# Optimization experiments

Hardware: AMD Instinct MI355X
Metric: run time of the kernel (lower is better)

## Reference

```python
import jax, jax.numpy as jnp
import numpy as np

E = 8          # num_experts
H = 2048       # hidden_size
I = 1408       # moe_intermediate_size
T = 4096       # tokens (batch*seq)
K = 2          # top_k


def setup_inputs() -> dict:
    key = jax.random.key(0)
    ks = jax.random.split(key, 6)
    hidden_states = jax.random.normal(ks[0], (T, H), dtype=jnp.float32)
    top_k_index = jax.random.randint(ks[1], (T, K), 0, E, dtype=jnp.int64)
    top_k_weights = jax.random.uniform(ks[2], (T, K), dtype=jnp.float32)
    scale = 0.02
    Wg = jax.random.normal(ks[3], (E, H, I), dtype=jnp.float32) * scale  # gate_proj per expert
    Wu = jax.random.normal(ks[4], (E, H, I), dtype=jnp.float32) * scale  # up_proj per expert
    Wd = jax.random.normal(ks[5], (E, I, H), dtype=jnp.float32) * scale  # down_proj per expert
    return {"hidden_states": hidden_states, "top_k_index": top_k_index,
            "top_k_weights": top_k_weights, "Wg": Wg, "Wu": Wu, "Wd": Wd}


def reference(hidden_states, top_k_index, top_k_weights, Wg, Wu, Wd):
    # Combine weights per (expert, token): w[e,t] = sum_k weights[t,k] * [idx[t,k]==e]
    one_hot = jax.nn.one_hot(top_k_index, E, dtype=hidden_states.dtype)  # [T,K,E]
    w = jnp.einsum('tke,tk->et', one_hot, top_k_weights)                 # [E,T]
    # SwiGLU MLP for every expert (dense masked-compute formulation of the
    # original gather->MLP->weighted scatter-add loop; identical math)
    g = jnp.einsum('th,ehi->eti', hidden_states, Wg)                     # [E,T,I]
    u = jnp.einsum('th,ehi->eti', hidden_states, Wu)                     # [E,T,I]
    y = jnp.einsum('eti,eih->eth', jax.nn.silu(g) * u, Wd)               # [E,T,H]
    # Weighted combine (scatter-add over experts)
    return jnp.einsum('et,eth->th', w, y)                                # [T,H]
```

## Files before the change

### kernel.cpp

```cpp
#include <hip/hip_runtime.h>

#define T_TOK 4096
#define H_DIM 2048
#define I_DIM 1408
#define E_NUM 8
#define NPAIR 8192
#define BM 128
#define BK 64

typedef float f32x4 __attribute__((ext_vector_type(4)));
typedef short s16x8 __attribute__((ext_vector_type(8)));

static __device__ __forceinline__ short f2bf(float f) {
  union { float f; unsigned u; } c; c.f = f;
  unsigned r = c.u + 0x7FFFu + ((c.u >> 16) & 1u);
  return (short)(r >> 16);
}

#define GLD16(g, l) __builtin_amdgcn_global_load_lds( \
    (const __attribute__((address_space(1))) void*)(g), \
    (__attribute__((address_space(3))) void*)(l), 16, 0, 0)

__global__ __launch_bounds__(256) void moe_build(
    const int* __restrict__ idx, const float* __restrict__ wts,
    int* __restrict__ tok_s, float* __restrict__ wt_s, int* __restrict__ inv,
    int* __restrict__ tile_e, int* __restrict__ tile_r0,
    int* __restrict__ tile_r1, int* __restrict__ ntiles) {
  __shared__ int cnt[E_NUM], cur[E_NUM];
  int tid = threadIdx.x;
  if (tid < E_NUM) cnt[tid] = 0;
  __syncthreads();
  for (int p = tid; p < NPAIR; p += 256) atomicAdd(&cnt[idx[p] & 7], 1);
  __syncthreads();
  if (tid == 0) {
    int o = 0, nt = 0;
    for (int e = 0; e < E_NUM; e++) {
      cur[e] = o;
      int c = cnt[e];
      for (int m0 = 0; m0 < c; m0 += BM) {
        tile_e[nt] = e;
        tile_r0[nt] = o + m0;
        tile_r1[nt] = o + ((m0 + BM < c) ? (m0 + BM) : c);
        nt++;
      }
      o += c;
    }
    *ntiles = nt;
  }
  __syncthreads();
  for (int p = tid; p < NPAIR; p += 256) {
    int e = idx[p] & 7;
    int pos = atomicAdd(&cur[e], 1);
    tok_s[pos] = p >> 1;
    wt_s[pos]  = wts[p];
    inv[p]     = pos;
  }
}

__global__ __launch_bounds__(256) void conv_hidden(
    const float* __restrict__ in, short* __restrict__ out) {
  size_t i = ((size_t)blockIdx.x * 256 + threadIdx.x) * 16;
  const f32x4* s = (const f32x4*)(in + i);
  f32x4 a = s[0], b = s[1], c = s[2], d = s[3];
  s16x8 v0, v1;
  v0[0]=f2bf(a[0]); v0[1]=f2bf(a[1]); v0[2]=f2bf(a[2]); v0[3]=f2bf(a[3]);
  v0[4]=f2bf(b[0]); v0[5]=f2bf(b[1]); v0[6]=f2bf(b[2]); v0[7]=f2bf(b[3]);
  v1[0]=f2bf(c[0]); v1[1]=f2bf(c[1]); v1[2]=f2bf(c[2]); v1[3]=f2bf(c[3]);
  v1[4]=f2bf(d[0]); v1[5]=f2bf(d[1]); v1[6]=f2bf(d[2]); v1[7]=f2bf(d[3]);
  *(s16x8*)(out + i) = v0;
  *(s16x8*)(out + i + 8) = v1;
}

__global__ __launch_bounds__(256) void transpose_w(
    const float* __restrict__ in, short* __restrict__ out, int R, int C) {
  __shared__ short t[64][72];
  const float* src = in + (size_t)blockIdx.z * ((size_t)R * C);
  short* dst = out + (size_t)blockIdx.z * ((size_t)R * C);
  int r0 = blockIdx.y * 64, c0 = blockIdx.x * 64;
  int tid = threadIdx.x;
  int ir = tid >> 2, ic = (tid & 3) * 16;
  const f32x4* s = (const f32x4*)(src + (size_t)(r0 + ir) * C + c0 + ic);
  f32x4 a = s[0], b = s[1], c = s[2], d = s[3];
  short* w = &t[ir][ic];
  w[0]=f2bf(a[0]);  w[1]=f2bf(a[1]);  w[2]=f2bf(a[2]);  w[3]=f2bf(a[3]);
  w[4]=f2bf(b[0]);  w[5]=f2bf(b[1]);  w[6]=f2bf(b[2]);  w[7]=f2bf(b[3]);
  w[8]=f2bf(c[0]);  w[9]=f2bf(c[1]);  w[10]=f2bf(c[2]); w[11]=f2bf(c[3]);
  w[12]=f2bf(d[0]); w[13]=f2bf(d[1]); w[14]=f2bf(d[2]); w[15]=f2bf(d[3]);
  __syncthreads();
  int oc = tid >> 2, os = (tid & 3) * 16;
  s16x8 v0, v1;
  #pragma unroll
  for (int j = 0; j < 8; j++) { v0[j] = t[os + j][oc]; v1[j] = t[os + 8 + j][oc]; }
  short* o = dst + (size_t)(c0 + oc) * R + r0 + os;
  *(s16x8*)o = v0;
  *(s16x8*)(o + 8) = v1;
}

__global__ __launch_bounds__(256, 2) void moe_gemm1(
    const short* __restrict__ hb, const short* __restrict__ Wgt,
    const short* __restrict__ Wut, const int* __restrict__ tok_s,
    const int* __restrict__ tile_e, const int* __restrict__ tile_r0,
    const int* __restrict__ tile_r1, const int* __restrict__ ntiles,
    short* __restrict__ act) {
  __shared__ short As[BM * BK];
  __shared__ short Bg[128 * BK];
  __shared__ short Bu[128 * BK];
  int bt = blockIdx.x;
  if (bt >= *ntiles) return;
  int e = tile_e[bt], r0 = tile_r0[bt], r1 = tile_r1[bt];
  int n0 = blockIdx.y * 128;
  const short* wg = Wgt + (size_t)e * ((size_t)H_DIM * I_DIM);
  const short* wu = Wut + (size_t)e * ((size_t)H_DIM * I_DIM);

  int tid = threadIdx.x, lane = tid & 63, wv = tid >> 6;
  int l3 = lane >> 3;
  int k8 = (((lane & 7) ^ l3) << 3);

  const short* a_src[4]; short* a_dst[4];
  const short* g_src[4]; short* g_dst[4];
  const short* u_src[4]; short* u_dst[4];
  #pragma unroll
  for (int s = 0; s < 4; s++) {
    int row = wv * 32 + s * 8 + l3;
    int p = r0 + row; if (p > NPAIR - 1) p = NPAIR - 1;
    a_src[s] = hb + (size_t)tok_s[p] * H_DIM + k8;
    a_dst[s] = As + (wv * 32 + s * 8) * BK;
    g_src[s] = wg + (size_t)(n0 + row) * H_DIM + k8;
    u_src[s] = wu + (size_t)(n0 + row) * H_DIM + k8;
    g_dst[s] = Bg + (wv * 32 + s * 8) * BK;
    u_dst[s] = Bu + (wv * 32 + s * 8) * BK;
  }

  int wm = wv >> 1, wn = wv & 1;
  int lrow = lane & 15, lk = lane >> 4;

  f32x4 accg[4][4], accu[4][4];
  #pragma unroll
  for (int i = 0; i < 4; i++)
    #pragma unroll
    for (int j = 0; j < 4; j++) { accg[i][j] = 0; accu[i][j] = 0; }

  for (int k0 = 0; k0 < H_DIM; k0 += BK) {
    #pragma unroll
    for (int s = 0; s < 4; s++) GLD16(a_src[s] + k0, a_dst[s]);
    #pragma unroll
    for (int s = 0; s < 4; s++) GLD16(g_src[s] + k0, g_dst[s]);
    #pragma unroll
    for (int s = 0; s < 4; s++) GLD16(u_src[s] + k0, u_dst[s]);
    __syncthreads();
    #pragma unroll
    for (int ks = 0; ks < 2; ks++) {
      s16x8 af[4], bgf[4], buf_[4];
      #pragma unroll
      for (int mf = 0; mf < 4; mf++) {
        int rr = wm * 64 + mf * 16 + lrow;
        af[mf] = *(const s16x8*)&As[rr * BK + ((((ks << 2) + lk) ^ (rr & 7)) << 3)];
      }
      #pragma unroll
      for (int nf = 0; nf < 4; nf++) {
        int rn = wn * 64 + nf * 16 + lrow;
        int o = rn * BK + ((((ks << 2) + lk) ^ (rn & 7)) << 3);
        bgf[nf] = *(const s16x8*)&Bg[o];
        buf_[nf] = *(const s16x8*)&Bu[o];
      }
      #pragma unroll
      for (int mf = 0; mf < 4; mf++)
        #pragma unroll
        for (int nf = 0; nf < 4; nf++) {
          accg[mf][nf] = __builtin_amdgcn_mfma_f32_16x16x32_bf16(af[mf], bgf[nf], accg[mf][nf], 0, 0, 0);
          accu[mf][nf] = __builtin_amdgcn_mfma_f32_16x16x32_bf16(af[mf], buf_[nf], accu[mf][nf], 0, 0, 0);
        }
    }
    __syncthreads();
  }
  #pragma unroll
  for (int mf = 0; mf < 4; mf++) {
    int rb = r0 + wm * 64 + mf * 16 + (lk << 2);
    #pragma unroll
    for (int nf = 0; nf < 4; nf++) {
      int col = n0 + wn * 64 + nf * 16 + lrow;
      #pragma unroll
      for (int j = 0; j < 4; j++) {
        int p = rb + j;
        if (p < r1) {
          float g = accg[mf][nf][j], u = accu[mf][nf][j];
          float s = g / (1.f + __expf(-g)) * u;
          act[p * I_DIM + col] = f2bf(s);
        }
      }
    }
  }
}

__global__ __launch_bounds__(256, 2) void moe_gemm2(
    const short* __restrict__ act, const short* __restrict__ Wdt,
    const int* __restrict__ tile_e, const int* __restrict__ tile_r0,
    const int* __restrict__ tile_r1, const int* __restrict__ ntiles,
    float* __restrict__ y) {
  __shared__ short As[BM * BK];
  __shared__ short Bd[128 * BK];
  int bt = blockIdx.x;
  if (bt >= *ntiles) return;
  int e = tile_e[bt], r0 = tile_r0[bt], r1 = tile_r1[bt];
  int n0 = blockIdx.y * 128;
  const short* wd = Wdt + (size_t)e * ((size_t)H_DIM * I_DIM);

  int tid = threadIdx.x, lane = tid & 63, wv = tid >> 6;
  int l3 = lane >> 3;
  int k8 = (((lane & 7) ^ l3) << 3);

  const short* a_src[4]; short* a_dst[4];
  const short* b_src[4]; short* b_dst[4];
  #pragma unroll
  for (int s = 0; s < 4; s++) {
    int row = wv * 32 + s * 8 + l3;
    int p = r0 + row; if (p > NPAIR - 1) p = NPAIR - 1;
    a_src[s] = act + (size_t)p * I_DIM + k8;
    a_dst[s] = As + (wv * 32 + s * 8) * BK;
    b_src[s] = wd + (size_t)(n0 + row) * I_DIM + k8;
    b_dst[s] = Bd + (wv * 32 + s * 8) * BK;
  }

  int wm = wv >> 1, wn = wv & 1;
  int lrow = lane & 15, lk = lane >> 4;

  f32x4 acc[4][4];
  #pragma unroll
  for (int i = 0; i < 4; i++)
    #pragma unroll
    for (int j = 0; j < 4; j++) acc[i][j] = 0;

  for (int k0 = 0; k0 < I_DIM; k0 += BK) {
    #pragma unroll
    for (int s = 0; s < 4; s++) GLD16(a_src[s] + k0, a_dst[s]);
    #pragma unroll
    for (int s = 0; s < 4; s++) GLD16(b_src[s] + k0, b_dst[s]);
    __syncthreads();
    #pragma unroll
    for (int ks = 0; ks < 2; ks++) {
      s16x8 af[4], bf[4];
      #pragma unroll
      for (int mf = 0; mf < 4; mf++) {
        int rr = wm * 64 + mf * 16 + lrow;
        af[mf] = *(const s16x8*)&As[rr * BK + ((((ks << 2) + lk) ^ (rr & 7)) << 3)];
      }
      #pragma unroll
      for (int nf = 0; nf < 4; nf++) {
        int rn = wn * 64 + nf * 16 + lrow;
        bf[nf] = *(const s16x8*)&Bd[rn * BK + ((((ks << 2) + lk) ^ (rn & 7)) << 3)];
      }
      #pragma unroll
      for (int mf = 0; mf < 4; mf++)
        #pragma unroll
        for (int nf = 0; nf < 4; nf++)
          acc[mf][nf] = __builtin_amdgcn_mfma_f32_16x16x32_bf16(af[mf], bf[nf], acc[mf][nf], 0, 0, 0);
    }
    __syncthreads();
  }
  #pragma unroll
  for (int mf = 0; mf < 4; mf++) {
    int rb = r0 + wm * 64 + mf * 16 + (lk << 2);
    #pragma unroll
    for (int nf = 0; nf < 4; nf++) {
      int col = n0 + wn * 64 + nf * 16 + lrow;
      #pragma unroll
      for (int j = 0; j < 4; j++) {
        int p = rb + j;
        if (p < r1) {
          y[(size_t)p * H_DIM + col] = acc[mf][nf][j];
        }
      }
    }
  }
}

__global__ __launch_bounds__(256) void moe_combine(
    const float* __restrict__ y, const int* __restrict__ inv,
    const float* __restrict__ wt_s, float* __restrict__ out) {
  int t = blockIdx.x;
  int p0 = inv[2 * t], p1 = inv[2 * t + 1];
  float w0 = wt_s[p0], w1 = wt_s[p1];
  const f32x4* y0 = (const f32x4*)(y + (size_t)p0 * H_DIM);
  const f32x4* y1 = (const f32x4*)(y + (size_t)p1 * H_DIM);
  f32x4* o = (f32x4*)(out + (size_t)t * H_DIM);
  int i = threadIdx.x;
  f32x4 a0 = y0[i], b0 = y1[i];
  f32x4 a1 = y0[i + 256], b1 = y1[i + 256];
  o[i] = w0 * a0 + w1 * b0;
  o[i + 256] = w0 * a1 + w1 * b1;
}

extern "C" void kernel_launch(void* const* d_in, const int* in_sizes, int n_in,
                              void* d_out, int out_size, void* d_ws, size_t ws_size,
                              hipStream_t stream) {
  const float* hidden = (const float*)d_in[0];
  const int*   idx    = (const int*)d_in[1];
  const float* wts    = (const float*)d_in[2];
  const float* Wg     = (const float*)d_in[3];
  const float* Wu     = (const float*)d_in[4];
  const float* Wd     = (const float*)d_in[5];
  float* out = (float*)d_out;

  char* ws = (char*)d_ws;
  int*   tok_s   = (int*)(ws);
  float* wt_s    = (float*)(ws + 32768);
  int*   tile_e  = (int*)(ws + 65536);
  int*   tile_r0 = (int*)(ws + 66048);
  int*   tile_r1 = (int*)(ws + 66560);
  int*   ntiles  = (int*)(ws + 67072);
  int*   inv     = (int*)(ws + 131072);

  const size_t OFF_HB  = 1ull << 20;
  const size_t OFF_WGT = OFF_HB  + 16777216ull;
  const size_t OFF_WUT = OFF_WGT + 46137344ull;
  const size_t OFF_WDT = OFF_WUT + 46137344ull;
  const size_t OFF_ACT = OFF_WDT + 46137344ull;

  short* hb  = (short*)(ws + OFF_HB);
  short* wgt = (short*)(ws + OFF_WGT);
  short* wut = (short*)(ws + OFF_WUT);
  short* wdt = (short*)(ws + OFF_WDT);
  short* act = (short*)(ws + OFF_ACT);
  float* y   = (float*)(ws + OFF_WGT);

  moe_build<<<1, 256, 0, stream>>>(idx, wts, tok_s, wt_s, inv, tile_e, tile_r0, tile_r1, ntiles);
  conv_hidden<<<2048, 256, 0, stream>>>(hidden, hb);
  transpose_w<<<dim3(I_DIM / 64, H_DIM / 64, E_NUM), 256, 0, stream>>>(Wg, wgt, H_DIM, I_DIM);
  transpose_w<<<dim3(I_DIM / 64, H_DIM / 64, E_NUM), 256, 0, stream>>>(Wu, wut, H_DIM, I_DIM);
  transpose_w<<<dim3(H_DIM / 64, I_DIM / 64, E_NUM), 256, 0, stream>>>(Wd, wdt, I_DIM, H_DIM);
  moe_gemm1<<<dim3(72, I_DIM / 128), 256, 0, stream>>>(hb, wgt, wut, tok_s,
      tile_e, tile_r0, tile_r1, ntiles, act);
  moe_gemm2<<<dim3(72, H_DIM / 128), 256, 0, stream>>>(act, wdt,
      tile_e, tile_r0, tile_r1, ntiles, y);
  moe_combine<<<T_TOK, 256, 0, stream>>>(y, inv, wt_s, out);
}
```

Measured before the change: 360.9 us.

## Double-buffer LDS tiles with BK=32 to overlap global loads with MFMA

Both expert GEMM kernels move from a single-buffered BK=64 loop with two __syncthreads per iteration to a double-buffered BK=32 pipeline. The next tile's global-to-LDS loads are issued before computing the current one, with explicit vmcnt waits and raw s_barrier calls. The LDS swizzle is redone for 32-wide rows, and s_setprio raises wave priority around the MFMA blocks. The aim is to hide global load latency behind compute. The cost is twice as many barrier rounds per K, and the hand-written waitcnt counts must match the number of issued loads.

Result: slower. 386.3 us (+7.0%).

```diff
diff --git a/kernel.cpp b/kernel.cpp
--- a/kernel.cpp
+++ b/kernel.cpp
@@ -6,7 +6,8 @@
 #define E_NUM 8
 #define NPAIR 8192
 #define BM 128
-#define BK 64
+#define NT1 64
+#define NT2 44
 
 typedef float f32x4 __attribute__((ext_vector_type(4)));
 typedef short s16x8 __attribute__((ext_vector_type(8)));
@@ -20,6 +21,8 @@
 #define GLD16(g, l) __builtin_amdgcn_global_load_lds( \
     (const __attribute__((address_space(1))) void*)(g), \
     (__attribute__((address_space(3))) void*)(l), 16, 0, 0)
+
+#define FENCE() asm volatile("" ::: "memory")
 
 __global__ __launch_bounds__(256) void moe_build(
     const int* __restrict__ idx, const float* __restrict__ wts,
@@ -102,9 +105,9 @@
     const int* __restrict__ tile_e, const int* __restrict__ tile_r0,
     const int* __restrict__ tile_r1, const int* __restrict__ ntiles,
     short* __restrict__ act) {
-  __shared__ short As[BM * BK];
-  __shared__ short Bg[128 * BK];
-  __shared__ short Bu[128 * BK];
+  __shared__ short As[2][128 * 32];
+  __shared__ short Bg[2][128 * 32];
+  __shared__ short Bu[2][128 * 32];
   int bt = blockIdx.x;
   if (bt >= *ntiles) return;
   int e = tile_e[bt], r0 = tile_r0[bt], r1 = tile_r1[bt];
@@ -113,26 +116,30 @@
   const short* wu = Wut + (size_t)e * ((size_t)H_DIM * I_DIM);
 
   int tid = threadIdx.x, lane = tid & 63, wv = tid >> 6;
-  int l3 = lane >> 3;
-  int k8 = (((lane & 7) ^ l3) << 3);
-
-  const short* a_src[4]; short* a_dst[4];
-  const short* g_src[4]; short* g_dst[4];
-  const short* u_src[4]; short* u_dst[4];
-  #pragma unroll
-  for (int s = 0; s < 4; s++) {
-    int row = wv * 32 + s * 8 + l3;
+  int lr16 = lane >> 2;
+  int gch = ((lane & 3) ^ ((lane >> 3) & 3)) << 3;
+
+  const short *a_src[2], *g_src[2], *u_src[2];
+  #pragma unroll
+  for (int s = 0; s < 2; s++) {
+    int row = wv * 32 + s * 16 + lr16;
     int p = r0 + row; if (p > NPAIR - 1) p = NPAIR - 1;
-    a_src[s] = hb + (size_t)tok_s[p] * H_DIM + k8;
-    a_dst[s] = As + (wv * 32 + s * 8) * BK;
-    g_src[s] = wg + (size_t)(n0 + row) * H_DIM + k8;
-    u_src[s] = wu + (size_t)(n0 + row) * H_DIM + k8;
-    g_dst[s] = Bg + (wv * 32 + s * 8) * BK;
-    u_dst[s] = Bu + (wv * 32 + s * 8) * BK;
-  }
+    a_src[s] = hb + (size_t)tok_s[p] * H_DIM + gch;
+    g_src[s] = wg + (size_t)(n0 + row) * H_DIM + gch;
+    u_src[s] = wu + (size_t)(n0 + row) * H_DIM + gch;
+  }
+  int d0 = (wv * 32) * 32, d1 = (wv * 32 + 16) * 32;
+
+  auto stage = [&](int b, int t) {
+    int k = t << 5;
+    GLD16(a_src[0] + k, &As[b][d0]); GLD16(a_src[1] + k, &As[b][d1]);
+    GLD16(g_src[0] + k, &Bg[b][d0]); GLD16(g_src[1] + k, &Bg[b][d1]);
+    GLD16(u_src[0] + k, &Bu[b][d0]); GLD16(u_src[1] + k, &Bu[b][d1]);
+  };
 
   int wm = wv >> 1, wn = wv & 1;
   int lrow = lane & 15, lk = lane >> 4;
+  int ch = (lk ^ ((lrow >> 1) & 3)) << 3;
 
   f32x4 accg[4][4], accu[4][4];
   #pragma unroll
@@ -140,39 +147,46 @@
     #pragma unroll
     for (int j = 0; j < 4; j++) { accg[i][j] = 0; accu[i][j] = 0; }
 
-  for (int k0 = 0; k0 < H_DIM; k0 += BK) {
-    #pragma unroll
-    for (int s = 0; s < 4; s++) GLD16(a_src[s] + k0, a_dst[s]);
-    #pragma unroll
-    for (int s = 0; s < 4; s++) GLD16(g_src[s] + k0, g_dst[s]);
-    #pragma unroll
-    for (int s = 0; s < 4; s++) GLD16(u_src[s] + k0, u_dst[s]);
-    __syncthreads();
-    #pragma unroll
-    for (int ks = 0; ks < 2; ks++) {
-      s16x8 af[4], bgf[4], buf_[4];
-      #pragma unroll
-      for (int mf = 0; mf < 4; mf++) {
-        int rr = wm * 64 + mf * 16 + lrow;
-        af[mf] = *(const s16x8*)&As[rr * BK + ((((ks << 2) + lk) ^ (rr & 7)) << 3)];
-      }
+  auto compute = [&](int b) {
+    s16x8 af[4], bgf[4], buf_[4];
+    #pragma unroll
+    for (int mf = 0; mf < 4; mf++)
+      af[mf] = *(const s16x8*)&As[b][(wm * 64 + mf * 16 + lrow) * 32 + ch];
+    #pragma unroll
+    for (int nf = 0; nf < 4; nf++) {
+      int o = (wn * 64 + nf * 16 + lrow) * 32 + ch;
+      bgf[nf] = *(const s16x8*)&Bg[b][o];
+      buf_[nf] = *(const s16x8*)&Bu[b][o];
+    }
+    __builtin_amdgcn_s_setprio(1);
+    #pragma unroll
+    for (int mf = 0; mf < 4; mf++)
       #pragma unroll
       for (int nf = 0; nf < 4; nf++) {
-        int rn = wn * 64 + nf * 16 + lrow;
-        int o = rn * BK + ((((ks << 2) + lk) ^ (rn & 7)) << 3);
-        bgf[nf] = *(const s16x8*)&Bg[o];
-        buf_[nf] = *(const s16x8*)&Bu[o];
+        accg[mf][nf] = __builtin_amdgcn_mfma_f32_16x16x32_bf16(af[mf], bgf[nf], accg[mf][nf], 0, 0, 0);
+        accu[mf][nf] = __builtin_amdgcn_mfma_f32_16x16x32_bf16(af[mf], buf_[nf], accu[mf][nf], 0, 0, 0);
       }
-      #pragma unroll
-      for (int mf = 0; mf < 4; mf++)
-        #pragma unroll
-        for (int nf = 0; nf < 4; nf++) {
-          accg[mf][nf] = __builtin_amdgcn_mfma_f32_16x16x32_bf16(af[mf], bgf[nf], accg[mf][nf], 0, 0, 0);
-          accu[mf][nf] = __builtin_amdgcn_mfma_f32_16x16x32_bf16(af[mf], buf_[nf], accu[mf][nf], 0, 0, 0);
-        }
-    }
-    __syncthreads();
-  }
+    __builtin_amdgcn_s_setprio(0);
+  };
+
+  stage(0, 0);
+  for (int t = 0; t < NT1 - 1; ++t) {
+    stage((t + 1) & 1, t + 1);
+    asm volatile("s_waitcnt vmcnt(6)" ::: "memory");
+    __builtin_amdgcn_sched_barrier(0);
+    __builtin_amdgcn_s_barrier();
+    FENCE();
+    compute(t & 1);
+    FENCE();
+    __builtin_amdgcn_s_barrier();
+    FENCE();
+  }
+  asm volatile("s_waitcnt vmcnt(0)" ::: "memory");
+  __builtin_amdgcn_sched_barrier(0);
+  __builtin_amdgcn_s_barrier();
+  FENCE();
+  compute((NT1 - 1) & 1);
+
   #pragma unroll
   for (int mf = 0; mf < 4; mf++) {
     int rb = r0 + wm * 64 + mf * 16 + (lk << 2);
@@ -197,8 +211,8 @@
     const int* __restrict__ tile_e, const int* __restrict__ tile_r0,
     const int* __restrict__ tile_r1, const int* __restrict__ ntiles,
     float* __restrict__ y) {
-  __shared__ short As[BM * BK];
-  __shared__ short Bd[128 * BK];
+  __shared__ short As[2][128 * 32];
+  __shared__ short Bd[2][128 * 32];
   int bt = blockIdx.x;
   if (bt >= *ntiles) return;
   int e = tile_e[bt], r0 = tile_r0[bt], r1 = tile_r1[bt];
@@ -206,23 +220,28 @@
   const short* wd = Wdt + (size_t)e * ((size_t)H_DIM * I_DIM);
 
   int tid = threadIdx.x, lane = tid & 63, wv = tid >> 6;
-  int l3 = lane >> 3;
-  int k8 = (((lane & 7) ^ l3) << 3);
-
-  const short* a_src[4]; short* a_dst[4];
-  const short* b_src[4]; short* b_dst[4];
-  #pragma unroll
-  for (int s = 0; s < 4; s++) {
-    int row = wv * 32 + s * 8 + l3;
+  int lr16 = lane >> 2;
+  int gch = ((lane & 3) ^ ((lane >> 3) & 3)) << 3;
+
+  const short *a_src[2], *b_src[2];
+  #pragma unroll
+  for (int s = 0; s < 2; s++) {
+    int row = wv * 32 + s * 16 + lr16;
     int p = r0 + row; if (p > NPAIR - 1) p = NPAIR - 1;
-    a_src[s] = act + (size_t)p * I_DIM + k8;
-    a_dst[s] = As + (wv * 32 + s * 8) * BK;
-    b_src[s] = wd + (size_t)(n0 + row) * I_DIM + k8;
-    b_dst[s] = Bd + (wv * 32 + s * 8) * BK;
-  }
+    a_src[s] = act + (size_t)p * I_DIM + gch;
+    b_src[s] = wd + (size_t)(n0 + row) * I_DIM + gch;
+  }
+  int d0 = (wv * 32) * 32, d1 = (wv * 32 + 16) * 32;
+
+  auto stage = [&](int b, int t) {
+    int k = t << 5;
+    GLD16(a_src[0] + k, &As[b][d0]); GLD16(a_src[1] + k, &As[b][d1]);
+    GLD16(b_src[0] + k, &Bd[b][d0]); GLD16(b_src[1] + k, &Bd[b][d1]);
+  };
 
   int wm = wv >> 1, wn = wv & 1;
   int lrow = lane & 15, lk = lane >> 4;
+  int ch = (lk ^ ((lrow >> 1) & 3)) << 3;
 
   f32x4 acc[4][4];
   #pragma unroll
@@ -230,33 +249,41 @@
     #pragma unroll
     for (int j = 0; j < 4; j++) acc[i][j] = 0;
 
-  for (int k0 = 0; k0 < I_DIM; k0 += BK) {
-    #pragma unroll
-    for (int s = 0; s < 4; s++) GLD16(a_src[s] + k0, a_dst[s]);
-    #pragma unroll
-    for (int s = 0; s < 4; s++) GLD16(b_src[s] + k0, b_dst[s]);
-    __syncthreads();
-    #pragma unroll
-    for (int ks = 0; ks < 2; ks++) {
-      s16x8 af[4], bf[4];
+  auto compute = [&](int b) {
+    s16x8 af[4], bf[4];
+    #pragma unroll
+    for (int mf = 0; mf < 4; mf++)
+      af[mf] = *(const s16x8*)&As[b][(wm * 64 + mf * 16 + lrow) * 32 + ch];
+    #pragma unroll
+    for (int nf = 0; nf < 4; nf++)
+      bf[nf] = *(const s16x8*)&Bd[b][(wn * 64 + nf * 16 + lrow) * 32 + ch];
+    __builtin_amdgcn_s_setprio(1);
+    #pragma unroll
+    for (int mf = 0; mf < 4; mf++)
       #pragma unroll
-      for (int mf = 0; mf < 4; mf++) {
-        int rr = wm * 64 + mf * 16 + lrow;
-        af[mf] = *(const s16x8*)&As[rr * BK + ((((ks << 2) + lk) ^ (rr & 7)) << 3)];
-      }
-      #pragma unroll
-      for (int nf = 0; nf < 4; nf++) {
-        int rn = wn * 64 + nf * 16 + lrow;
-        bf[nf] = *(const s16x8*)&Bd[rn * BK + ((((ks << 2) + lk) ^ (rn & 7)) << 3)];
-      }
-      #pragma unroll
-      for (int mf = 0; mf < 4; mf++)
-        #pragma unroll
-        for (int nf = 0; nf < 4; nf++)
-          acc[mf][nf] = __builtin_amdgcn_mfma_f32_16x16x32_bf16(af[mf], bf[nf], acc[mf][nf], 0, 0, 0);
-    }
-    __syncthreads();
-  }
+      for (int nf = 0; nf < 4; nf++)
+        acc[mf][nf] = __builtin_amdgcn_mfma_f32_16x16x32_bf16(af[mf], bf[nf], acc[mf][nf], 0, 0, 0);
+    __builtin_amdgcn_s_setprio(0);
+  };
+
+  stage(0, 0);
+  for (int t = 0; t < NT2 - 1; ++t) {
+    stage((t + 1) & 1, t + 1);
+    asm volatile("s_waitcnt vmcnt(4)" ::: "memory");
+    __builtin_amdgcn_sched_barrier(0);
+    __builtin_amdgcn_s_barrier();
+    FENCE();
+    compute(t & 1);
+    FENCE();
+    __builtin_amdgcn_s_barrier();
+    FENCE();
+  }
+  asm volatile("s_waitcnt vmcnt(0)" ::: "memory");
+  __builtin_amdgcn_sched_barrier(0);
+  __builtin_amdgcn_s_barrier();
+  FENCE();
+  compute((NT2 - 1) & 1);
+
   #pragma unroll
   for (int mf = 0; mf < 4; mf++) {
     int rb = r0 + wm * 64 + mf * 16 + (lk << 2);
```

## Fuse prep kernels into one launch and overlap GEMM tile loads with MFMA

Applied to the files above, without the earlier changes.

Merges the routing build, hidden-state conversion and three weight transposes into a single grid-partitioned prep kernel, removing four launches and letting the single-block build run alongside the conversion work. Both expert GEMMs are restructured so the second half-K fragments are read into registers, the next tile's global-to-LDS loads are issued, and then the remaining MFMAs run while those loads are in flight. This hides part of the load latency but keeps a single LDS buffer, so two barriers per iteration remain, and register pressure rises from holding both fragment sets.

New measurement: 336.2 us. -6.8%, faster.

```diff
diff --git a/kernel.cpp b/kernel.cpp
--- a/kernel.cpp
+++ b/kernel.cpp
@@ -7,6 +7,8 @@
 #define NPAIR 8192
 #define BM 128
 #define BK 64
+#define NT1 32
+#define NT2 22
 
 typedef float f32x4 __attribute__((ext_vector_type(4)));
 typedef short s16x8 __attribute__((ext_vector_type(8)));
@@ -21,69 +23,78 @@
     (const __attribute__((address_space(1))) void*)(g), \
     (__attribute__((address_space(3))) void*)(l), 16, 0, 0)
 
-__global__ __launch_bounds__(256) void moe_build(
+__global__ __launch_bounds__(256) void moe_prep(
+    const float* __restrict__ hidden, const float* __restrict__ Wg,
+    const float* __restrict__ Wu, const float* __restrict__ Wd,
     const int* __restrict__ idx, const float* __restrict__ wts,
+    short* __restrict__ hb, short* __restrict__ wgt,
+    short* __restrict__ wut, short* __restrict__ wdt,
     int* __restrict__ tok_s, float* __restrict__ wt_s, int* __restrict__ inv,
     int* __restrict__ tile_e, int* __restrict__ tile_r0,
     int* __restrict__ tile_r1, int* __restrict__ ntiles) {
+  __shared__ short t[64][72];
   __shared__ int cnt[E_NUM], cur[E_NUM];
-  int tid = threadIdx.x;
-  if (tid < E_NUM) cnt[tid] = 0;
-  __syncthreads();
-  for (int p = tid; p < NPAIR; p += 256) atomicAdd(&cnt[idx[p] & 7], 1);
-  __syncthreads();
-  if (tid == 0) {
-    int o = 0, nt = 0;
-    for (int e = 0; e < E_NUM; e++) {
-      cur[e] = o;
-      int c = cnt[e];
-      for (int m0 = 0; m0 < c; m0 += BM) {
-        tile_e[nt] = e;
-        tile_r0[nt] = o + m0;
-        tile_r1[nt] = o + ((m0 + BM < c) ? (m0 + BM) : c);
-        nt++;
+  int b = blockIdx.x, tid = threadIdx.x;
+
+  if (b < 2048) {
+    size_t i = ((size_t)b * 256 + tid) * 16;
+    const f32x4* s = (const f32x4*)(hidden + i);
+    f32x4 a = s[0], bb = s[1], c = s[2], d = s[3];
+    s16x8 v0, v1;
+    v0[0]=f2bf(a[0]); v0[1]=f2bf(a[1]); v0[2]=f2bf(a[2]); v0[3]=f2bf(a[3]);
+    v0[4]=f2bf(bb[0]); v0[5]=f2bf(bb[1]); v0[6]=f2bf(bb[2]); v0[7]=f2bf(bb[3]);
+    v1[0]=f2bf(c[0]); v1[1]=f2bf(c[1]); v1[2]=f2bf(c[2]); v1[3]=f2bf(c[3]);
+    v1[4]=f2bf(d[0]); v1[5]=f2bf(d[1]); v1[6]=f2bf(d[2]); v1[7]=f2bf(d[3]);
+    *(s16x8*)(hb + i) = v0;
+    *(s16x8*)(hb + i + 8) = v1;
+    return;
+  }
+  if (b == 18944) {
+    if (tid < E_NUM) cnt[tid] = 0;
+    __syncthreads();
+    for (int p = tid; p < NPAIR; p += 256) atomicAdd(&cnt[idx[p] & 7], 1);
+    __syncthreads();
+    if (tid == 0) {
+      int o = 0, nt = 0;
+      for (int e = 0; e < E_NUM; e++) {
+        cur[e] = o;
+        int c = cnt[e];
+        for (int m0 = 0; m0 < c; m0 += BM) {
+          tile_e[nt] = e;
+          tile_r0[nt] = o + m0;
+          tile_r1[nt] = o + ((m0 + BM < c) ? (m0 + BM) : c);
+          nt++;
+        }
+        o += c;
       }
-      o += c;
+      *ntiles = nt;
     }
-    *ntiles = nt;
-  }
-  __syncthreads();
-  for (int p = tid; p < NPAIR; p += 256) {
-    int e = idx[p] & 7;
-    int pos = atomicAdd(&cur[e], 1);
-    tok_s[pos] = p >> 1;
-    wt_s[pos]  = wts[p];
-    inv[p]     = pos;
-  }
-}
-
-__global__ __launch_bounds__(256) void conv_hidden(
-    const float* __restrict__ in, short* __restrict__ out) {
-  size_t i = ((size_t)blockIdx.x * 256 + threadIdx.x) * 16;
-  const f32x4* s = (const f32x4*)(in + i);
-  f32x4 a = s[0], b = s[1], c = s[2], d = s[3];
-  s16x8 v0, v1;
-  v0[0]=f2bf(a[0]); v0[1]=f2bf(a[1]); v0[2]=f2bf(a[2]); v0[3]=f2bf(a[3]);
-  v0[4]=f2bf(b[0]); v0[5]=f2bf(b[1]); v0[6]=f2bf(b[2]); v0[7]=f2bf(b[3]);
-  v1[0]=f2bf(c[0]); v1[1]=f2bf(c[1]); v1[2]=f2bf(c[2]); v1[3]=f2bf(c[3]);
-  v1[4]=f2bf(d[0]); v1[5]=f2bf(d[1]); v1[6]=f2bf(d[2]); v1[7]=f2bf(d[3]);
-  *(s16x8*)(out + i) = v0;
-  *(s16x8*)(out + i + 8) = v1;
-}
-
-__global__ __launch_bounds__(256) void transpose_w(
-    const float* __restrict__ in, short* __restrict__ out, int R, int C) {
-  __shared__ short t[64][72];
-  const float* src = in + (size_t)blockIdx.z * ((size_t)R * C);
-  short* dst = out + (size_t)blockIdx.z * ((size_t)R * C);
-  int r0 = blockIdx.y * 64, c0 = blockIdx.x * 64;
-  int tid = threadIdx.x;
+    __syncthreads();
+    for (int p = tid; p < NPAIR; p += 256) {
+      int e = idx[p] & 7;
+      int pos = atomicAdd(&cur[e], 1);
+      tok_s[pos] = p >> 1;
+      wt_s[pos]  = wts[p];
+      inv[p]     = pos;
+    }
+    return;
+  }
+  const float* src; short* dst; int R, C, lb;
+  if (b < 7680)       { src = Wg; dst = wgt; R = H_DIM; C = I_DIM; lb = b - 2048; }
+  else if (b < 13312) { src = Wu; dst = wut; R = H_DIM; C = I_DIM; lb = b - 7680; }
+  else                { src = Wd; dst = wdt; R = I_DIM; C = H_DIM; lb = b - 13312; }
+  int ncx = C >> 6, nry = R >> 6;
+  int cx = lb % ncx, tmp = lb / ncx;
+  int ry = tmp % nry, ez = tmp / nry;
+  src += (size_t)ez * ((size_t)R * C);
+  dst += (size_t)ez * ((size_t)R * C);
+  int r0 = ry * 64, c0 = cx * 64;
   int ir = tid >> 2, ic = (tid & 3) * 16;
   const f32x4* s = (const f32x4*)(src + (size_t)(r0 + ir) * C + c0 + ic);
-  f32x4 a = s[0], b = s[1], c = s[2], d = s[3];
+  f32x4 a = s[0], bb = s[1], c = s[2], d = s[3];
   short* w = &t[ir][ic];
   w[0]=f2bf(a[0]);  w[1]=f2bf(a[1]);  w[2]=f2bf(a[2]);  w[3]=f2bf(a[3]);
-  w[4]=f2bf(b[0]);  w[5]=f2bf(b[1]);  w[6]=f2bf(b[2]);  w[7]=f2bf(b[3]);
+  w[4]=f2bf(bb[0]); w[5]=f2bf(bb[1]); w[6]=f2bf(bb[2]); w[7]=f2bf(bb[3]);
   w[8]=f2bf(c[0]);  w[9]=f2bf(c[1]);  w[10]=f2bf(c[2]); w[11]=f2bf(c[3]);
   w[12]=f2bf(d[0]); w[13]=f2bf(d[1]); w[14]=f2bf(d[2]); w[15]=f2bf(d[3]);
   __syncthreads();
@@ -103,8 +114,8 @@
     const int* __restrict__ tile_r1, const int* __restrict__ ntiles,
     short* __restrict__ act) {
   __shared__ short As[BM * BK];
-  __shared__ short Bg[128 * BK];
-  __shared__ short Bu[128 * BK];
+  __shared__ short Bg[BM * BK];
+  __shared__ short Bu[BM * BK];
   int bt = blockIdx.x;
   if (bt >= *ntiles) return;
   int e = tile_e[bt], r0 = tile_r0[bt], r1 = tile_r1[bt];
@@ -116,23 +127,24 @@
   int l3 = lane >> 3;
   int k8 = (((lane & 7) ^ l3) << 3);
 
-  const short* a_src[4]; short* a_dst[4];
-  const short* g_src[4]; short* g_dst[4];
-  const short* u_src[4]; short* u_dst[4];
+  const short *a_src[4], *g_src[4], *u_src[4];
+  short *a_dst[4], *g_dst[4], *u_dst[4];
   #pragma unroll
   for (int s = 0; s < 4; s++) {
     int row = wv * 32 + s * 8 + l3;
     int p = r0 + row; if (p > NPAIR - 1) p = NPAIR - 1;
     a_src[s] = hb + (size_t)tok_s[p] * H_DIM + k8;
-    a_dst[s] = As + (wv * 32 + s * 8) * BK;
     g_src[s] = wg + (size_t)(n0 + row) * H_DIM + k8;
     u_src[s] = wu + (size_t)(n0 + row) * H_DIM + k8;
+    a_dst[s] = As + (wv * 32 + s * 8) * BK;
     g_dst[s] = Bg + (wv * 32 + s * 8) * BK;
     u_dst[s] = Bu + (wv * 32 + s * 8) * BK;
   }
 
   int wm = wv >> 1, wn = wv & 1;
   int lrow = lane & 15, lk = lane >> 4;
+  int ch0 = ((lk ^ (lrow & 7)) << 3);
+  int ch1 = (((4 + lk) ^ (lrow & 7)) << 3);
 
   f32x4 accg[4][4], accu[4][4];
   #pragma unroll
@@ -140,39 +152,55 @@
     #pragma unroll
     for (int j = 0; j < 4; j++) { accg[i][j] = 0; accu[i][j] = 0; }
 
-  for (int k0 = 0; k0 < H_DIM; k0 += BK) {
-    #pragma unroll
-    for (int s = 0; s < 4; s++) GLD16(a_src[s] + k0, a_dst[s]);
-    #pragma unroll
-    for (int s = 0; s < 4; s++) GLD16(g_src[s] + k0, g_dst[s]);
-    #pragma unroll
-    for (int s = 0; s < 4; s++) GLD16(u_src[s] + k0, u_dst[s]);
-    __syncthreads();
-    #pragma unroll
-    for (int ks = 0; ks < 2; ks++) {
-      s16x8 af[4], bgf[4], buf_[4];
-      #pragma unroll
-      for (int mf = 0; mf < 4; mf++) {
-        int rr = wm * 64 + mf * 16 + lrow;
-        af[mf] = *(const s16x8*)&As[rr * BK + ((((ks << 2) + lk) ^ (rr & 7)) << 3)];
-      }
-      #pragma unroll
-      for (int nf = 0; nf < 4; nf++) {
-        int rn = wn * 64 + nf * 16 + lrow;
-        int o = rn * BK + ((((ks << 2) + lk) ^ (rn & 7)) << 3);
-        bgf[nf] = *(const s16x8*)&Bg[o];
-        buf_[nf] = *(const s16x8*)&Bu[o];
-      }
-      #pragma unroll
-      for (int mf = 0; mf < 4; mf++)
-        #pragma unroll
-        for (int nf = 0; nf < 4; nf++) {
-          accg[mf][nf] = __builtin_amdgcn_mfma_f32_16x16x32_bf16(af[mf], bgf[nf], accg[mf][nf], 0, 0, 0);
-          accu[mf][nf] = __builtin_amdgcn_mfma_f32_16x16x32_bf16(af[mf], buf_[nf], accu[mf][nf], 0, 0, 0);
-        }
-    }
-    __syncthreads();
-  }
+  #define G1_STAGE(t) do { int kk = (t) << 6; \
+    GLD16(a_src[0]+kk, a_dst[0]); GLD16(a_src[1]+kk, a_dst[1]); \
+    GLD16(a_src[2]+kk, a_dst[2]); GLD16(a_src[3]+kk, a_dst[3]); \
+    GLD16(g_src[0]+kk, g_dst[0]); GLD16(g_src[1]+kk, g_dst[1]); \
+    GLD16(g_src[2]+kk, g_dst[2]); GLD16(g_src[3]+kk, g_dst[3]); \
+    GLD16(u_src[0]+kk, u_dst[0]); GLD16(u_src[1]+kk, u_dst[1]); \
+    GLD16(u_src[2]+kk, u_dst[2]); GLD16(u_src[3]+kk, u_dst[3]); } while (0)
+
+  #define G1_RD(ch, af, bgf, buf_) do { \
+    _Pragma("unroll") \
+    for (int mf = 0; mf < 4; mf++) \
+      af[mf] = *(const s16x8*)&As[(wm * 64 + mf * 16 + lrow) * BK + (ch)]; \
+    _Pragma("unroll") \
+    for (int nf = 0; nf < 4; nf++) { \
+      int oo = (wn * 64 + nf * 16 + lrow) * BK + (ch); \
+      bgf[nf] = *(const s16x8*)&Bg[oo]; \
+      buf_[nf] = *(const s16x8*)&Bu[oo]; } } while (0)
+
+  #define G1_MFMA(af, bgf, buf_) do { \
+    _Pragma("unroll") \
+    for (int mf = 0; mf < 4; mf++) \
+      _Pragma("unroll") \
+      for (int nf = 0; nf < 4; nf++) { \
+        accg[mf][nf] = __builtin_amdgcn_mfma_f32_16x16x32_bf16(af[mf], bgf[nf], accg[mf][nf], 0, 0, 0); \
+        accu[mf][nf] = __builtin_amdgcn_mfma_f32_16x16x32_bf16(af[mf], buf_[nf], accu[mf][nf], 0, 0, 0); } } while (0)
+
+  G1_STAGE(0);
+  __syncthreads();
+  for (int t = 0; t < NT1 - 1; ++t) {
+    s16x8 a0[4], bg0[4], bu0[4];
+    G1_RD(ch0, a0, bg0, bu0);
+    G1_MFMA(a0, bg0, bu0);
+    s16x8 a1[4], bg1[4], bu1[4];
+    G1_RD(ch1, a1, bg1, bu1);
+    __syncthreads();
+    G1_STAGE(t + 1);
+    __builtin_amdgcn_sched_barrier(0);
+    G1_MFMA(a1, bg1, bu1);
+    __syncthreads();
+  }
+  {
+    s16x8 a0[4], bg0[4], bu0[4];
+    G1_RD(ch0, a0, bg0, bu0);
+    G1_MFMA(a0, bg0, bu0);
+    s16x8 a1[4], bg1[4], bu1[4];
+    G1_RD(ch1, a1, bg1, bu1);
+    G1_MFMA(a1, bg1, bu1);
+  }
+
   #pragma unroll
   for (int mf = 0; mf < 4; mf++) {
     int rb = r0 + wm * 64 + mf * 16 + (lk << 2);
@@ -198,7 +226,7 @@
     const int* __restrict__ tile_r1, const int* __restrict__ ntiles,
     float* __restrict__ y) {
   __shared__ short As[BM * BK];
-  __shared__ short Bd[128 * BK];
+  __shared__ short Bd[BM * BK];
   int bt = blockIdx.x;
   if (bt >= *ntiles) return;
   int e = tile_e[bt], r0 = tile_r0[bt], r1 = tile_r1[bt];
@@ -209,20 +237,22 @@
   int l3 = lane >> 3;
   int k8 = (((lane & 7) ^ l3) << 3);
 
-  const short* a_src[4]; short* a_dst[4];
-  const short* b_src[4]; short* b_dst[4];
+  const short *a_src[4], *b_src[4];
+  short *a_dst[4], *b_dst[4];
   #pragma unroll
   for (int s = 0; s < 4; s++) {
     int row = wv * 32 + s * 8 + l3;
     int p = r0 + row; if (p > NPAIR - 1) p = NPAIR - 1;
     a_src[s] = act + (size_t)p * I_DIM + k8;
+    b_src[s] = wd + (size_t)(n0 + row) * I_DIM + k8;
     a_dst[s] = As + (wv * 32 + s * 8) * BK;
-    b_src[s] = wd + (size_t)(n0 + row) * I_DIM + k8;
     b_dst[s] = Bd + (wv * 32 + s * 8) * BK;
   }
 
   int wm = wv >> 1, wn = wv & 1;
   int lrow = lane & 15, lk = lane >> 4;
+  int ch0 = ((lk ^ (lrow & 7)) << 3);
+  int ch1 = (((4 + lk) ^ (lrow & 7)) << 3);
 
   f32x4 acc[4][4];
   #pragma unroll
@@ -230,33 +260,50 @@
     #pragma unroll
     for (int j = 0; j < 4; j++) acc[i][j] = 0;
 
-  for (int k0 = 0; k0 < I_DIM; k0 += BK) {
-    #pragma unroll
-    for (int s = 0; s < 4; s++) GLD16(a_src[s] + k0, a_dst[s]);
-    #pragma unroll
-    for (int s = 0; s < 4; s++) GLD16(b_src[s] + k0, b_dst[s]);
-    __syncthreads();
-    #pragma unroll
-    for (int ks = 0; ks < 2; ks++) {
-      s16x8 af[4], bf[4];
-      #pragma unroll
-      for (int mf = 0; mf < 4; mf++) {
-        int rr = wm * 64 + mf * 16 + lrow;
-        af[mf] = *(const s16x8*)&As[rr * BK + ((((ks << 2) + lk) ^ (rr & 7)) << 3)];
-      }
-      #pragma unroll
-      for (int nf = 0; nf < 4; nf++) {
-        int rn = wn * 64 + nf * 16 + lrow;
-        bf[nf] = *(const s16x8*)&Bd[rn * BK + ((((ks << 2) + lk) ^ (rn & 7)) << 3)];
-      }
-      #pragma unroll
-      for (int mf = 0; mf < 4; mf++)
-        #pragma unroll
-        for (int nf = 0; nf < 4; nf++)
-          acc[mf][nf] = __builtin_amdgcn_mfma_f32_16x16x32_bf16(af[mf], bf[nf], acc[mf][nf], 0, 0, 0);
-    }
-    __syncthreads();
-  }
+  #define G2_STAGE(t) do { int kk = (t) << 6; \
+    GLD16(a_src[0]+kk, a_dst[0]); GLD16(a_src[1]+kk, a_dst[1]); \
+    GLD16(a_src[2]+kk, a_dst[2]); GLD16(a_src[3]+kk, a_dst[3]); \
+    GLD16(b_src[0]+kk, b_dst[0]); GLD16(b_src[1]+kk, b_dst[1]); \
+    GLD16(b_src[2]+kk, b_dst[2]); GLD16(b_src[3]+kk, b_dst[3]); } while (0)
+
+  #define G2_RD(ch, af, bf) do { \
+    _Pragma("unroll") \
+    for (int mf = 0; mf < 4; mf++) \
+      af[mf] = *(const s16x8*)&As[(wm * 64 + mf * 16 + lrow) * BK + (ch)]; \
+    _Pragma("unroll") \
+    for (int nf = 0; nf < 4; nf++) \
+      bf[nf] = *(const s16x8*)&Bd[(wn * 64 + nf * 16 + lrow) * BK + (ch)]; } while (0)
+
+  #define G2_MFMA(af, bf) do { \
+    _Pragma("unroll") \
+    for (int mf = 0; mf < 4; mf++) \
+      _Pragma("unroll") \
+      for (int nf = 0; nf < 4; nf++) \
+        acc[mf][nf] = __builtin_amdgcn_mfma_f32_16x16x32_bf16(af[mf], bf[nf], acc[mf][nf], 0, 0, 0); } while (0)
+
+  G2_STAGE(0);
+  __syncthreads();
+  for (int t = 0; t < NT2 - 1; ++t) {
+    s16x8 a0[4], b0[4];
+    G2_RD(ch0, a0, b0);
+    G2_MFMA(a0, b0);
+    s16x8 a1[4], b1[4];
+    G2_RD(ch1, a1, b1);
+    __syncthreads();
+    G2_STAGE(t + 1);
+    __builtin_amdgcn_sched_barrier(0);
+    G2_MFMA(a1, b1);
+    __syncthreads();
+  }
+  {
+    s16x8 a0[4], b0[4];
+    G2_RD(ch0, a0, b0);
+    G2_MFMA(a0, b0);
+    s16x8 a1[4], b1[4];
+    G2_RD(ch1, a1, b1);
+    G2_MFMA(a1, b1);
+  }
+
   #pragma unroll
   for (int mf = 0; mf < 4; mf++) {
     int rb = r0 + wm * 64 + mf * 16 + (lk << 2);
@@ -323,11 +370,8 @@
   short* act = (short*)(ws + OFF_ACT);
   float* y   = (float*)(ws + OFF_WGT);
 
-  moe_build<<<1, 256, 0, stream>>>(idx, wts, tok_s, wt_s, inv, tile_e, tile_r0, tile_r1, ntiles);
-  conv_hidden<<<2048, 256, 0, stream>>>(hidden, hb);
-  transpose_w<<<dim3(I_DIM / 64, H_DIM / 64, E_NUM), 256, 0, stream>>>(Wg, wgt, H_DIM, I_DIM);
-  transpose_w<<<dim3(I_DIM / 64, H_DIM / 64, E_NUM), 256, 0, stream>>>(Wu, wut, H_DIM, I_DIM);
-  transpose_w<<<dim3(H_DIM / 64, I_DIM / 64, E_NUM), 256, 0, stream>>>(Wd, wdt, I_DIM, H_DIM);
+  moe_prep<<<18945, 256, 0, stream>>>(hidden, Wg, Wu, Wd, idx, wts,
+      hb, wgt, wut, wdt, tok_s, wt_s, inv, tile_e, tile_r0, tile_r1, ntiles);
   moe_gemm1<<<dim3(72, I_DIM / 128), 256, 0, stream>>>(hb, wgt, wut, tok_s,
       tile_e, tile_r0, tile_r1, ntiles, act);
   moe_gemm2<<<dim3(72, H_DIM / 128), 256, 0, stream>>>(act, wdt,
```
